# Kernel optimization log

Measured on AMD Instinct MI355X. Metric: run time of the kernel, lower is better.

The kernel has to match this reference:

```python
import jax, jax.numpy as jnp
import numpy as np
from jax import lax
import math

B, T, CIN, H, W = 8, 64, 2, 64, 64
HID, SPK_C = 32, 64
D_MODEL, N_LAYERS, D_STATE, D_CONV = 512, 4, 16, 4
D_INNER = 2 * D_MODEL
DT_RANK = math.ceil(D_MODEL / 16)  # 32
NUM_CLASSES = 11
FEAT = SPK_C * (H // 4) * (W // 4)  # 16384
BETA, THR = 0.9, 1.0

# --- surrogate-gradient spike (snntorch fast_sigmoid, slope=25) ---
@jax.custom_vjp
def spike_fn(x):
    return (x > 0).astype(x.dtype)

def _spike_fwd(x):
    return spike_fn(x), x

def _spike_bwd(x, g):
    return (g / (25.0 * jnp.abs(x) + 1.0) ** 2,)

spike_fn.defvjp(_spike_fwd, _spike_bwd)

def lif(cur, mem):
    # snntorch Leaky, reset_mechanism='subtract': reset from previous mem (detached)
    reset = lax.stop_gradient((mem > THR).astype(mem.dtype))
    mem = BETA * mem + cur - reset * THR
    spk = spike_fn(mem - THR)
    return spk, mem

def conv2d(x, w, b):
    y = lax.conv_general_dilated(x, w, (1, 1), 'SAME', dimension_numbers=('NCHW', 'OIHW', 'NCHW'))
    return y + b[None, :, None, None]

def maxpool2(x):
    return lax.reduce_window(x, -jnp.inf, lax.max, (1, 1, 2, 2), (1, 1, 2, 2), 'VALID')

def layernorm(x, w, b):
    mu = x.mean(-1, keepdims=True)
    var = ((x - mu) ** 2).mean(-1, keepdims=True)
    return (x - mu) * lax.rsqrt(var + 1e-5) * w + b

def frontend(x, c1w, c1b, c2w, c2b, c3w, c3b):
    mem1 = jnp.zeros((B, HID, H // 2, W // 2), x.dtype)
    mem2 = jnp.zeros((B, HID, H // 4, W // 4), x.dtype)
    mem3 = jnp.zeros((B, SPK_C, H // 4, W // 4), x.dtype)
    def step(carry, xt):
        m1, m2, m3 = carry
        s1, m1 = lif(maxpool2(conv2d(xt, c1w, c1b)), m1)
        s2, m2 = lif(maxpool2(conv2d(s1, c2w, c2b)), m2)
        s3, m3 = lif(conv2d(s2, c3w, c3b), m3)
        return (m1, m2, m3), s3
    _, spk = lax.scan(step, (mem1, mem2, mem3), jnp.swapaxes(x, 0, 1))
    return jnp.swapaxes(spk, 0, 1)  # (B,T,SPK_C,H/4,W/4)

def rate_smooth(a):
    # depthwise conv1d over time with kernel ones(5)/5, padding=2 (moving average)
    Tn = a.shape[1]
    ap = jnp.pad(a, ((0, 0), (2, 2), (0, 0)))
    return sum(ap[:, k:k + Tn, :] for k in range(5)) / 5.0

def mamba_block(x, p):
    ln_w, ln_b, in_w, conv_w, xproj_w, dt_w, dt_b, A_log, Dp, out_w = p
    h = layernorm(x, ln_w, ln_b)
    xr = h @ in_w  # (B,L,2*D_INNER)
    xi, res = jnp.split(xr, 2, axis=-1)
    L = xi.shape[1]
    # causal depthwise conv1d (pad D_CONV-1 left, truncate to L)
    xp = jnp.pad(xi, ((0, 0), (D_CONV - 1, 0), (0, 0)))
    xc = sum(conv_w[:, k] * xp[:, k:k + L, :] for k in range(D_CONV))
    xc = jax.nn.silu(xc)
    x_dbl = xc @ xproj_w  # (B,L,DT_RANK+2*D_STATE)
    dt = x_dbl[..., :DT_RANK]
    Bm = x_dbl[..., DT_RANK:DT_RANK + D_STATE]
    Cm = x_dbl[..., DT_RANK + D_STATE:]
    dt = jax.nn.softplus(dt @ dt_w + dt_b)  # (B,L,D_INNER)
    A = -jnp.exp(A_log)  # (D_INNER,D_STATE)
    dA = jnp.exp(dt[..., None] * A)  # (B,L,D_INNER,D_STATE)
    dBu = dt[..., None] * Bm[:, :, None, :] * xc[..., None]
    def step(hst, inp):
        dA_t, dBu_t, C_t = inp
        hst = dA_t * hst + dBu_t
        return hst, jnp.einsum('bdn,bn->bd', hst, C_t)
    h0 = jnp.zeros((x.shape[0], D_INNER, D_STATE), x.dtype)
    _, ys = lax.scan(step, h0, (jnp.swapaxes(dA, 0, 1), jnp.swapaxes(dBu, 0, 1), jnp.swapaxes(Cm, 0, 1)))
    y = jnp.swapaxes(ys, 0, 1) + xc * Dp
    y = y * jax.nn.silu(res)
    return x + y @ out_w

def _forward(x, c1w, c1b, c2w, c2b, c3w, c3b, inp_w, inp_b, ln_w, ln_b, in_w, conv_w, xproj_w, dt_w, dt_b, A_log, Dp, mb_out_w, fn_w, fn_b, cls_w, cls_b):
    spikes = frontend(x, c1w, c1b, c2w, c2b, c3w, c3b)
    act = rate_smooth(spikes.reshape(B, T, -1))
    h = act @ inp_w + inp_b
    def layer(c, p):
        return mamba_block(c, p), None
    h, _ = lax.scan(layer, h, (ln_w, ln_b, in_w, conv_w, xproj_w, dt_w, dt_b, A_log, Dp, mb_out_w))
    h = h.mean(axis=1)
    h = layernorm(h, fn_w, fn_b)
    return h @ cls_w + cls_b

def setup_inputs():
    key = jax.random.key(0)
    ks = jax.random.split(key, 16)
    def gn(k, shape, scale):
        return jax.random.normal(k, shape, jnp.float32) * scale
    x = jax.random.uniform(ks[0], (B, T, CIN, H, W), jnp.float32)
    c1w = gn(ks[1], (HID, CIN, 3, 3), 1.0 / np.sqrt(CIN * 9)); c1b = jnp.zeros((HID,))
    c2w = gn(ks[2], (HID, HID, 3, 3), 1.0 / np.sqrt(HID * 9)); c2b = jnp.zeros((HID,))
    c3w = gn(ks[3], (SPK_C, HID, 3, 3), 1.0 / np.sqrt(HID * 9)); c3b = jnp.zeros((SPK_C,))
    inp_w = gn(ks[4], (FEAT, D_MODEL), 1.0 / np.sqrt(FEAT)); inp_b = jnp.zeros((D_MODEL,))
    ln_w = jnp.ones((N_LAYERS, D_MODEL)); ln_b = jnp.zeros((N_LAYERS, D_MODEL))
    in_w = gn(ks[5], (N_LAYERS, D_MODEL, 2 * D_INNER), 1.0 / np.sqrt(D_MODEL))
    conv_w = gn(ks[6], (N_LAYERS, D_INNER, D_CONV), 1.0 / np.sqrt(D_CONV))
    xproj_w = gn(ks[7], (N_LAYERS, D_INNER, DT_RANK + 2 * D_STATE), 1.0 / np.sqrt(D_INNER))
    dt_w = gn(ks[8], (N_LAYERS, DT_RANK, D_INNER), 1.0 / np.sqrt(DT_RANK))
    dtv = jnp.exp(jax.random.uniform(ks[9], (N_LAYERS, D_INNER)) * (np.log(0.1) - np.log(0.001)) + np.log(0.001))
    dt_b = dtv + jnp.log(-jnp.expm1(-dtv))
    A_log = jnp.log(jnp.broadcast_to(jnp.arange(1, D_STATE + 1, dtype=jnp.float32), (N_LAYERS, D_INNER, D_STATE))) + jnp.zeros((N_LAYERS, D_INNER, D_STATE))
    Dp = jnp.ones((N_LAYERS, D_INNER))
    mb_out_w = gn(ks[10], (N_LAYERS, D_INNER, D_MODEL), 1.0 / np.sqrt(D_INNER))
    fn_w = jnp.ones((D_MODEL,)); fn_b = jnp.zeros((D_MODEL,))
    cls_w = gn(ks[11], (D_MODEL, NUM_CLASSES), 1.0 / np.sqrt(D_MODEL)); cls_b = jnp.zeros((NUM_CLASSES,))
    return dict(x=x, c1w=c1w, c1b=c1b, c2w=c2w, c2b=c2b, c3w=c3w, c3b=c3b, inp_w=inp_w, inp_b=inp_b, ln_w=ln_w, ln_b=ln_b, in_w=in_w, conv_w=conv_w, xproj_w=xproj_w, dt_w=dt_w, dt_b=dt_b, A_log=A_log, Dp=Dp, mb_out_w=mb_out_w, fn_w=fn_w, fn_b=fn_b, cls_w=cls_w, cls_b=cls_b)

def reference(x, c1w, c1b, c2w, c2b, c3w, c3b, inp_w, inp_b, ln_w, ln_b, in_w, conv_w, xproj_w, dt_w, dt_b, A_log, Dp, mb_out_w, fn_w, fn_b, cls_w, cls_b):
    return _forward(x, c1w, c1b, c2w, c2b, c3w, c3b, inp_w, inp_b, ln_w, ln_b, in_w, conv_w, xproj_w, dt_w, dt_b, A_log, Dp, mb_out_w, fn_w, fn_b, cls_w, cls_b)
```

## Files before the change

### kernel.cpp

```cpp
#include <hip/hip_runtime.h>
#include <math.h>


static constexpr int TT = 64;
static constexpr float BETA = 0.9f, THR = 1.0f;


__global__ __launch_bounds__(256) void k_conv1pool(const float* __restrict__ x,
    const float* __restrict__ w, const float* __restrict__ bias, float* __restrict__ out)
{
    __shared__ float sI[2 * 66 * 76];
    __shared__ float sW[576];
    const int bt = blockIdx.x;
    const int tid = threadIdx.x;
    for (int i = tid; i < 2 * 66 * 76; i += 256) sI[i] = 0.f;
    for (int i = tid; i < 576; i += 256) sW[i] = w[i];
    __syncthreads();
    const float* img = x + (size_t)bt * 8192;
    for (int i = tid; i < 2048; i += 256) {
        float4 v4 = ((const float4*)img)[i];
        int lin = i * 4;
        int ci = lin >> 12, rc = lin & 4095;
        int r = rc >> 6, c = rc & 63;
        *(float4*)&sI[ci * 5016 + (r + 1) * 76 + (c + 4)] = v4;
    }
    __syncthreads();
    const int oh = tid >> 3;
    const int p8 = (tid & 7) * 8;
    float v[2][4][10];
    #pragma unroll
    for (int ci = 0; ci < 2; ++ci) {
        #pragma unroll
        for (int dr = 0; dr < 4; ++dr) {
            const float* rp = &sI[ci * 5016 + (2 * oh + dr) * 76 + p8];
            float2 a  = *(const float2*)&rp[2];
            float4 b4 = *(const float4*)&rp[4];
            float4 c4 = *(const float4*)&rp[8];
            float2 e  = *(const float2*)&rp[12];
            v[ci][dr][0] = a.y;
            v[ci][dr][1] = b4.x; v[ci][dr][2] = b4.y; v[ci][dr][3] = b4.z; v[ci][dr][4] = b4.w;
            v[ci][dr][5] = c4.x; v[ci][dr][6] = c4.y; v[ci][dr][7] = c4.z; v[ci][dr][8] = c4.w;
            v[ci][dr][9] = e.x;
        }
    }
    const int ow0 = (tid & 7) * 4;
    float* obase = out + (size_t)bt * 32768;
    for (int co = 0; co < 32; ++co) {
        float pos[2][8];
        #pragma unroll
        for (int i = 0; i < 2; ++i)
            #pragma unroll
            for (int j = 0; j < 8; ++j) pos[i][j] = 0.f;
        #pragma unroll
        for (int ci = 0; ci < 2; ++ci) {
            const float* wp = &sW[(co * 2 + ci) * 9];
            float w0=wp[0],w1=wp[1],w2=wp[2],w3=wp[3],w4=wp[4],w5=wp[5],w6=wp[6],w7=wp[7],w8=wp[8];
            #pragma unroll
            for (int pr = 0; pr < 2; ++pr)
                #pragma unroll
                for (int pc = 0; pc < 8; ++pc)
                    pos[pr][pc] += v[ci][pr][pc]*w0 + v[ci][pr][pc+1]*w1 + v[ci][pr][pc+2]*w2
                                 + v[ci][pr+1][pc]*w3 + v[ci][pr+1][pc+1]*w4 + v[ci][pr+1][pc+2]*w5
                                 + v[ci][pr+2][pc]*w6 + v[ci][pr+2][pc+1]*w7 + v[ci][pr+2][pc+2]*w8;
        }
        float b0 = bias[co];
        float4 o;
        o.x = fmaxf(fmaxf(pos[0][0], pos[0][1]), fmaxf(pos[1][0], pos[1][1])) + b0;
        o.y = fmaxf(fmaxf(pos[0][2], pos[0][3]), fmaxf(pos[1][2], pos[1][3])) + b0;
        o.z = fmaxf(fmaxf(pos[0][4], pos[0][5]), fmaxf(pos[1][4], pos[1][5])) + b0;
        o.w = fmaxf(fmaxf(pos[0][6], pos[0][7]), fmaxf(pos[1][6], pos[1][7])) + b0;
        *(float4*)&obase[co * 1024 + oh * 32 + ow0] = o;
    }
}

__global__ __launch_bounds__(256) void k_lif(const float* __restrict__ cur,
                                             float* __restrict__ spk, int chw)
{
    int idx = blockIdx.x * 256 + threadIdx.x;
    int b = idx / chw, p = idx % chw;
    const float* cp = cur + (size_t)b * TT * chw + p;
    float* sp = spk + (size_t)b * TT * chw + p;
    float m = 0.f;
    for (int t = 0; t < TT; ++t) {
        float c = cp[(size_t)t * chw];
        float reset = (m > THR) ? THR : 0.f;
        m = BETA * m + c - reset;
        sp[(size_t)t * chw] = (m > THR) ? 1.f : 0.f;
    }
}

__global__ __launch_bounds__(256) void k_conv2(const float* __restrict__ s1,
    const float* __restrict__ w, const float* __restrict__ bias, float* __restrict__ out)
{
    __shared__ float sI[8 * 34 * 40];
    __shared__ float sWc[576];
    const int bt = blockIdx.x;
    const int co0 = blockIdx.y * 8;
    const int tid = threadIdx.x;
    for (int i = tid; i < 8 * 34 * 40; i += 256) sI[i] = 0.f;
    const int cop = (tid >> 6) * 2;
    const int lane = tid & 63;
    const int ph0 = (lane >> 3) * 4;
    const int pw0 = (lane & 7) * 4;
    float acc[2][4][4] = {};
    const float* img = s1 + (size_t)bt * 32768;
    for (int chunk = 0; chunk < 4; ++chunk) {
        __syncthreads();
        const float* src = img + chunk * 8192;
        for (int i = tid; i < 2048; i += 256) {
            float4 v4 = ((const float4*)src)[i];
            int lin = i * 4;
            int ci = lin >> 10, rc = lin & 1023;
            int r = rc >> 5, c = rc & 31;
            *(float4*)&sI[ci * 1360 + (r + 1) * 40 + (c + 4)] = v4;
        }
        for (int i = tid; i < 576; i += 256) {
            int col = i / 72, rest = i % 72;
            sWc[i] = w[(co0 + col) * 288 + chunk * 72 + rest];
        }
        __syncthreads();
        #pragma unroll
        for (int ci = 0; ci < 8; ++ci) {
            float wA[9], wB[9];
            #pragma unroll
            for (int j = 0; j < 9; ++j) {
                wA[j] = sWc[cop * 72 + ci * 9 + j];
                wB[j] = sWc[(cop + 1) * 72 + ci * 9 + j];
            }
            const float* sp = &sI[ci * 1360];
            float v[6][6];
            #pragma unroll
            for (int r6 = 0; r6 < 6; ++r6) {
                const float* rp = sp + (ph0 + r6) * 40 + pw0;
                float2 a  = *(const float2*)&rp[2];
                float4 b4 = *(const float4*)&rp[4];
                float2 e  = *(const float2*)&rp[8];
                v[r6][0] = a.y;
                v[r6][1] = b4.x; v[r6][2] = b4.y; v[r6][3] = b4.z; v[r6][4] = b4.w;
                v[r6][5] = e.x;
            }
            #pragma unroll
            for (int i = 0; i < 4; ++i)
                #pragma unroll
                for (int j = 0; j < 4; ++j) {
                    acc[0][i][j] += v[i][j]*wA[0] + v[i][j+1]*wA[1] + v[i][j+2]*wA[2]
                                  + v[i+1][j]*wA[3] + v[i+1][j+1]*wA[4] + v[i+1][j+2]*wA[5]
                                  + v[i+2][j]*wA[6] + v[i+2][j+1]*wA[7] + v[i+2][j+2]*wA[8];
                    acc[1][i][j] += v[i][j]*wB[0] + v[i][j+1]*wB[1] + v[i][j+2]*wB[2]
                                  + v[i+1][j]*wB[3] + v[i+1][j+1]*wB[4] + v[i+1][j+2]*wB[5]
                                  + v[i+2][j]*wB[6] + v[i+2][j+1]*wB[7] + v[i+2][j+2]*wB[8];
                }
        }
    }
    #pragma unroll
    for (int u = 0; u < 2; ++u) {
        int co = co0 + cop + u;
        float b0 = bias[co];
        float* ob = out + (size_t)bt * 8192 + co * 256;
        #pragma unroll
        for (int i = 0; i < 2; ++i) {
            float2 o;
            o.x = fmaxf(fmaxf(acc[u][2*i][0], acc[u][2*i][1]),
                        fmaxf(acc[u][2*i+1][0], acc[u][2*i+1][1])) + b0;
            o.y = fmaxf(fmaxf(acc[u][2*i][2], acc[u][2*i][3]),
                        fmaxf(acc[u][2*i+1][2], acc[u][2*i+1][3])) + b0;
            *(float2*)&ob[(ph0 / 2 + i) * 16 + pw0 / 2] = o;
        }
    }
}

__global__ __launch_bounds__(256) void k_conv3(const float* __restrict__ s2,
    const float* __restrict__ w, const float* __restrict__ bias, float* __restrict__ out)
{
    __shared__ float sI[32 * 16 * 17];
    __shared__ float sW[32 * 16 * 9];
    const int bt = blockIdx.x;
    const int co0 = blockIdx.y * 32;
    const int tid = threadIdx.x;
    const float* img = s2 + (size_t)bt * 8192;
    for (int i = tid; i < 2048; i += 256) {
        float4 v4 = ((const float4*)img)[i];
        int lin = i * 4;
        int ci = lin >> 8, rc = lin & 255;
        int r = rc >> 4, c = rc & 15;
        float* dst = &sI[ci * 272 + r * 17 + c];
        dst[0] = v4.x; dst[1] = v4.y; dst[2] = v4.z; dst[3] = v4.w;
    }
    const int cop = (tid >> 4) * 2;
    const int l16 = tid & 15;
    const int ph0 = (l16 >> 2) * 4;
    const int pw0 = (l16 & 3) * 4;
    float acc[2][4][4] = {};
    for (int chunk = 0; chunk < 2; ++chunk) {
        __syncthreads();
        for (int i = tid; i < 4608; i += 256) {
            int col = i / 144;
            int rest = i % 144;
            sW[i] = w[((co0 + col) * 32 + chunk * 16) * 9 + rest];
        }
        __syncthreads();
        for (int ci = 0; ci < 16; ++ci) {
            float v[6][6];
            const float* sp = &sI[(chunk * 16 + ci) * 272];
            #pragma unroll
            for (int dr = 0; dr < 6; ++dr) {
                int r = ph0 - 1 + dr;
                bool rok = (r >= 0) && (r < 16);
                #pragma unroll
                for (int dc = 0; dc < 6; ++dc) {
                    int c = pw0 - 1 + dc;
                    v[dr][dc] = (rok && c >= 0 && c < 16) ? sp[r * 17 + c] : 0.f;
                }
            }
            #pragma unroll
            for (int u = 0; u < 2; ++u) {
                const float* wp = &sW[((cop + u) * 16 + ci) * 9];
                float w0=wp[0],w1=wp[1],w2=wp[2],w3=wp[3],w4=wp[4],w5=wp[5],w6=wp[6],w7=wp[7],w8=wp[8];
                #pragma unroll
                for (int i = 0; i < 4; ++i)
                    #pragma unroll
                    for (int j = 0; j < 4; ++j)
                        acc[u][i][j] += v[i][j]*w0 + v[i][j+1]*w1 + v[i][j+2]*w2
                                      + v[i+1][j]*w3 + v[i+1][j+1]*w4 + v[i+1][j+2]*w5
                                      + v[i+2][j]*w6 + v[i+2][j+1]*w7 + v[i+2][j+2]*w8;
            }
        }
    }
    #pragma unroll
    for (int u = 0; u < 2; ++u) {
        int co = co0 + cop + u;
        float b0 = bias[co];
        float* ob = out + (size_t)bt * 16384 + co * 256;
        #pragma unroll
        for (int i = 0; i < 4; ++i) {
            float4 o;
            o.x = acc[u][i][0] + b0; o.y = acc[u][i][1] + b0;
            o.z = acc[u][i][2] + b0; o.w = acc[u][i][3] + b0;
            *(float4*)&ob[(ph0 + i) * 16 + pw0] = o;
        }
    }
}

__global__ __launch_bounds__(256) void k_lif3smooth(const float* __restrict__ cur,
                                                    float* __restrict__ act)
{
    int idx = blockIdx.x * 256 + threadIdx.x;
    int b = idx >> 14, f = idx & 16383;
    const float* cp = cur + (size_t)b * TT * 16384 + f;
    float* ap = act + (size_t)b * TT * 16384 + f;
    float m = 0.f;
    float s0 = 0, s1 = 0, s2 = 0, s3 = 0, s4 = 0;
    for (int t = 0; t < TT + 2; ++t) {
        float s = 0.f;
        if (t < TT) {
            float cv = cp[(size_t)t * 16384];
            float reset = (m > THR) ? THR : 0.f;
            m = BETA * m + cv - reset;
            s = (m > THR) ? 1.f : 0.f;
        }
        s4 = s3; s3 = s2; s2 = s1; s1 = s0; s0 = s;
        if (t >= 2) ap[(size_t)(t - 2) * 16384] = (s0 + s1 + s2 + s3 + s4) * 0.2f;
    }
}


__global__ __launch_bounds__(256) void k_gemm(const float* __restrict__ A,
    const float* __restrict__ Bm, float* __restrict__ C, int M, int N, int K)
{
    __shared__ float As[16][68];
    __shared__ float Bs[16][68];
    const int tid = threadIdx.x;
    const int n0 = blockIdx.x * 64, m0 = blockIdx.y * 64;
    const int kchunk = K / gridDim.z;
    const int k0 = blockIdx.z * kchunk, k1 = k0 + kchunk;
    const int ar = tid >> 2, ac = (tid & 3) * 4;
    const int br = tid >> 4, bc = (tid & 15) * 4;
    const int row0 = (tid >> 4) * 4, col0 = (tid & 15) * 4;
    float acc[4][4] = {};
    float4 av = *(const float4*)&A[(size_t)(m0 + ar) * K + k0 + ac];
    float4 bv = *(const float4*)&Bm[(size_t)(k0 + br) * N + n0 + bc];
    for (int kk = k0; kk < k1; kk += 16) {
        As[ac + 0][ar] = av.x; As[ac + 1][ar] = av.y;
        As[ac + 2][ar] = av.z; As[ac + 3][ar] = av.w;
        *(float4*)&Bs[br][bc] = bv;
        __syncthreads();
        if (kk + 16 < k1) {
            av = *(const float4*)&A[(size_t)(m0 + ar) * K + kk + 16 + ac];
            bv = *(const float4*)&Bm[(size_t)(kk + 16 + br) * N + n0 + bc];
        }
        #pragma unroll
        for (int k = 0; k < 16; ++k) {
            float4 a4 = *(const float4*)&As[k][row0];
            float4 b4 = *(const float4*)&Bs[k][col0];
            acc[0][0] += a4.x * b4.x; acc[0][1] += a4.x * b4.y; acc[0][2] += a4.x * b4.z; acc[0][3] += a4.x * b4.w;
            acc[1][0] += a4.y * b4.x; acc[1][1] += a4.y * b4.y; acc[1][2] += a4.y * b4.z; acc[1][3] += a4.y * b4.w;
            acc[2][0] += a4.z * b4.x; acc[2][1] += a4.z * b4.y; acc[2][2] += a4.z * b4.z; acc[2][3] += a4.z * b4.w;
            acc[3][0] += a4.w * b4.x; acc[3][1] += a4.w * b4.y; acc[3][2] += a4.w * b4.z; acc[3][3] += a4.w * b4.w;
        }
        __syncthreads();
    }
    float* Cp = C + (size_t)blockIdx.z * M * N;
    #pragma unroll
    for (int i = 0; i < 4; ++i) {
        float4 o;
        o.x = acc[i][0]; o.y = acc[i][1]; o.z = acc[i][2]; o.w = acc[i][3];
        *(float4*)&Cp[(size_t)(m0 + row0 + i) * N + n0 + col0] = o;
    }
}

template <bool ADD, bool BIAS>
__global__ __launch_bounds__(256) void k_reduce(const float* __restrict__ part,
    const float* __restrict__ bias, float* __restrict__ out, int MN, int N, int KS)
{
    int i4 = (blockIdx.x * 256 + threadIdx.x) * 4;
    if (i4 >= MN) return;
    float4 v = {0.f, 0.f, 0.f, 0.f};
    for (int z = 0; z < KS; ++z) {
        float4 p = *(const float4*)&part[(size_t)z * MN + i4];
        v.x += p.x; v.y += p.y; v.z += p.z; v.w += p.w;
    }
    if (BIAS) {
        float4 bv = *(const float4*)&bias[i4 % N];
        v.x += bv.x; v.y += bv.y; v.z += bv.z; v.w += bv.w;
    }
    if (ADD) {
        float4 o = *(const float4*)&out[i4];
        v.x += o.x; v.y += o.y; v.z += o.z; v.w += o.w;
    }
    *(float4*)&out[i4] = v;
}


__device__ __forceinline__ float blockSum(float v, float* red)
{
    #pragma unroll
    for (int o = 32; o; o >>= 1) v += __shfl_down(v, o, 64);
    const int wv = threadIdx.x >> 6, lane = threadIdx.x & 63;
    if (lane == 0) red[wv] = v;
    __syncthreads();
    float r = red[0] + red[1] + red[2] + red[3];
    __syncthreads();
    return r;
}

__global__ __launch_bounds__(256) void k_ln(const float* __restrict__ x,
    const float* __restrict__ w, const float* __restrict__ b, float* __restrict__ out)
{
    __shared__ float red[4];
    int row = blockIdx.x;
    const float* xp = x + (size_t)row * 512;
    int c = threadIdx.x * 2;
    float2 v = *(const float2*)&xp[c];
    float mu = blockSum(v.x + v.y, red) * (1.f / 512.f);
    float d0 = v.x - mu, d1 = v.y - mu;
    float var = blockSum(d0 * d0 + d1 * d1, red) * (1.f / 512.f);
    float inv = rsqrtf(var + 1e-5f);
    float2 o;
    o.x = d0 * inv * w[c] + b[c];
    o.y = d1 * inv * w[c + 1] + b[c + 1];
    *(float2*)&out[(size_t)row * 512 + c] = o;
}

__global__ __launch_bounds__(256) void k_convsilu(const float* __restrict__ xr,
    const float* __restrict__ cw, float* __restrict__ xc)
{
    int idx = blockIdx.x * 256 + threadIdx.x;
    int row = idx >> 10;
    int d = idx & 1023;
    int t = row & 63;
    const float* xi = xr + (size_t)(row - t) * 2048 + d;
    float4 w = *(const float4*)&cw[d * 4];
    float a = w.w * xi[(size_t)t * 2048];
    if (t >= 1) a += w.z * xi[(size_t)(t - 1) * 2048];
    if (t >= 2) a += w.y * xi[(size_t)(t - 2) * 2048];
    if (t >= 3) a += w.x * xi[(size_t)(t - 3) * 2048];
    xc[idx] = a / (1.f + __expf(-a));
}

__global__ __launch_bounds__(256) void k_xproj(const float* __restrict__ xc,
    const float* __restrict__ w, float* __restrict__ xdbl)
{
    int row = blockIdx.x * 4 + (threadIdx.x >> 6);
    int col = threadIdx.x & 63;
    const float* a = xc + (size_t)row * 1024;
    float acc = 0.f;
    #pragma unroll 4
    for (int k = 0; k < 1024; k += 4) {
        float4 av = *(const float4*)&a[k];
        acc += av.x * w[(size_t)k * 64 + col] + av.y * w[(size_t)(k + 1) * 64 + col]
             + av.z * w[(size_t)(k + 2) * 64 + col] + av.w * w[(size_t)(k + 3) * 64 + col];
    }
    xdbl[(size_t)row * 64 + col] = acc;
}

__global__ __launch_bounds__(256) void k_dtproj(const float* __restrict__ xdbl,
    const float* __restrict__ w, const float* __restrict__ bias, float* __restrict__ dt)
{
    int idx = blockIdx.x * 256 + threadIdx.x;
    int row = idx >> 10, d = idx & 1023;
    const float* a = xdbl + (size_t)row * 64;
    float acc = bias[d];
    #pragma unroll 8
    for (int r = 0; r < 32; ++r) acc += a[r] * w[(size_t)r * 1024 + d];
    dt[idx] = fmaxf(acc, 0.f) + log1pf(__expf(-fabsf(acc)));
}

__global__ __launch_bounds__(64) void k_scan(const float* __restrict__ dt,
    const float* __restrict__ xc, const float* __restrict__ xdbl,
    const float* __restrict__ xr, const float* __restrict__ A_log,
    const float* __restrict__ Dp, float* __restrict__ y)
{
    int idx = blockIdx.x * 64 + threadIdx.x;
    int b = idx >> 10, d = idx & 1023;
    float A[16];
    #pragma unroll
    for (int n = 0; n < 16; ++n) A[n] = -__expf(A_log[d * 16 + n]);
    float Dv = Dp[d];
    float h[16] = {};
    const int row0 = b * 64;
    size_t base = (size_t)row0 * 1024 + d;
    float dtv = dt[base], xv = xc[base];
    float res = xr[(size_t)row0 * 2048 + 1024 + d];
    const float4* Bp = (const float4*)&xdbl[(size_t)row0 * 64 + 32];
    const float4* Cq = (const float4*)&xdbl[(size_t)row0 * 64 + 48];
    float4 B0 = Bp[0], B1 = Bp[1], B2 = Bp[2], B3 = Bp[3];
    float4 C0 = Cq[0], C1 = Cq[1], C2 = Cq[2], C3 = Cq[3];
    for (int t = 0; t < TT; ++t) {
        float dtv_n = 0.f, xv_n = 0.f, res_n = 0.f;
        float4 B0n = {}, B1n = {}, B2n = {}, B3n = {}, C0n = {}, C1n = {}, C2n = {}, C3n = {};
        if (t < TT - 1) {
            size_t b2 = base + (size_t)(t + 1) * 1024;
            dtv_n = dt[b2]; xv_n = xc[b2];
            res_n = xr[(size_t)(row0 + t + 1) * 2048 + 1024 + d];
            const float4* Bp2 = (const float4*)&xdbl[(size_t)(row0 + t + 1) * 64 + 32];
            const float4* Cq2 = (const float4*)&xdbl[(size_t)(row0 + t + 1) * 64 + 48];
            B0n = Bp2[0]; B1n = Bp2[1]; B2n = Bp2[2]; B3n = Bp2[3];
            C0n = Cq2[0]; C1n = Cq2[1]; C2n = Cq2[2]; C3n = Cq2[3];
        }
        float dtx = dtv * xv;
        float acc = 0.f;
        #define SCAN_STEP(Bv, Cv, n0)                                             \
        {                                                                         \
            float bb[4] = {Bv.x, Bv.y, Bv.z, Bv.w};                               \
            float cv[4] = {Cv.x, Cv.y, Cv.z, Cv.w};                               \
            _Pragma("unroll")                                                     \
            for (int r = 0; r < 4; ++r) {                                         \
                int n = n0 + r;                                                   \
                float hv = __expf(dtv * A[n]) * h[n] + dtx * bb[r];               \
                h[n] = hv;                                                        \
                acc += hv * cv[r];                                                \
            }                                                                     \
        }
        SCAN_STEP(B0, C0, 0) SCAN_STEP(B1, C1, 4) SCAN_STEP(B2, C2, 8) SCAN_STEP(B3, C3, 12)
        #undef SCAN_STEP
        float sil = res / (1.f + __expf(-res));
        y[(size_t)(row0 + t) * 1024 + d] = (acc + xv * Dv) * sil;
        dtv = dtv_n; xv = xv_n; res = res_n;
        B0 = B0n; B1 = B1n; B2 = B2n; B3 = B3n;
        C0 = C0n; C1 = C1n; C2 = C2n; C3 = C3n;
    }
}

__global__ __launch_bounds__(256) void k_meant(const float* __restrict__ h,
                                               float* __restrict__ hm)
{
    int idx = blockIdx.x * 256 + threadIdx.x;
    int b = idx >> 9, d = idx & 511;
    const float* p = h + (size_t)b * 64 * 512 + d;
    float s = 0.f;
    for (int t = 0; t < 64; ++t) s += p[t * 512];
    hm[idx] = s * (1.f / 64.f);
}

__global__ __launch_bounds__(256) void k_final(const float* __restrict__ hm,
    const float* __restrict__ fw, const float* __restrict__ fb,
    const float* __restrict__ cw, const float* __restrict__ cb, float* __restrict__ out)
{
    __shared__ float red[4];
    __shared__ float nrm[512];
    int b = blockIdx.x;
    const float* xp = hm + (size_t)b * 512;
    int c2 = threadIdx.x * 2;
    float2 v = *(const float2*)&xp[c2];
    float mu = blockSum(v.x + v.y, red) * (1.f / 512.f);
    float d0 = v.x - mu, d1 = v.y - mu;
    float var = blockSum(d0 * d0 + d1 * d1, red) * (1.f / 512.f);
    float inv = rsqrtf(var + 1e-5f);
    nrm[c2] = d0 * inv * fw[c2] + fb[c2];
    nrm[c2 + 1] = d1 * inv * fw[c2 + 1] + fb[c2 + 1];
    __syncthreads();
    for (int c = 0; c < 11; ++c) {
        float p = nrm[threadIdx.x] * cw[threadIdx.x * 11 + c]
                + nrm[threadIdx.x + 256] * cw[(threadIdx.x + 256) * 11 + c];
        float s = blockSum(p, red);
        if (threadIdx.x == 0) out[b * 11 + c] = s + cb[c];
    }
}


extern "C" void kernel_launch(void* const* d_in, const int* in_sizes, int n_in,
                              void* d_out, int out_size, void* d_ws, size_t ws_size,
                              hipStream_t stream)
{
    const float* x      = (const float*)d_in[0];
    const float* c1w    = (const float*)d_in[1];
    const float* c1b    = (const float*)d_in[2];
    const float* c2w    = (const float*)d_in[3];
    const float* c2b    = (const float*)d_in[4];
    const float* c3w    = (const float*)d_in[5];
    const float* c3b    = (const float*)d_in[6];
    const float* inp_w  = (const float*)d_in[7];
    const float* inp_b  = (const float*)d_in[8];
    const float* ln_w   = (const float*)d_in[9];
    const float* ln_b   = (const float*)d_in[10];
    const float* in_w   = (const float*)d_in[11];
    const float* conv_w = (const float*)d_in[12];
    const float* xproj_w= (const float*)d_in[13];
    const float* dt_w   = (const float*)d_in[14];
    const float* dt_b   = (const float*)d_in[15];
    const float* A_log  = (const float*)d_in[16];
    const float* Dp     = (const float*)d_in[17];
    const float* mb_out_w=(const float*)d_in[18];
    const float* fn_w   = (const float*)d_in[19];
    const float* fn_b   = (const float*)d_in[20];
    const float* cls_w  = (const float*)d_in[21];
    const float* cls_b  = (const float*)d_in[22];
    float* out = (float*)d_out;

    float* ws   = (float*)d_ws;
    float* bufA = ws;
    float* bufB = bufA + 16777216;
    float* h    = bufB + 16777216;
    float* hn   = h    + 262144;
    float* xr   = hn   + 262144;
    float* xc   = xr   + 1048576;
    float* xdbl = xc   + 524288;
    float* dtb  = xdbl + 32768;
    float* yb   = dtb  + 524288;
    float* hm   = yb   + 524288;

    k_conv1pool<<<512, 256, 0, stream>>>(x, c1w, c1b, bufA);
    k_lif<<<1024, 256, 0, stream>>>(bufA, bufB, 32768);
    k_conv2<<<dim3(512, 4), 256, 0, stream>>>(bufB, c2w, c2b, bufA);
    k_lif<<<256, 256, 0, stream>>>(bufA, bufB, 8192);
    k_conv3<<<dim3(512, 2), 256, 0, stream>>>(bufB, c3w, c3b, bufA);
    k_lif3smooth<<<512, 256, 0, stream>>>(bufA, bufB);

    k_gemm<<<dim3(8, 8, 32), 256, 0, stream>>>(bufB, inp_w, bufA, 512, 512, 16384);
    k_reduce<false, true><<<256, 256, 0, stream>>>(bufA, inp_b, h, 262144, 512, 32);

    for (int l = 0; l < 4; ++l) {
        k_ln<<<512, 256, 0, stream>>>(h, ln_w + l * 512, ln_b + l * 512, hn);
        k_gemm<<<dim3(32, 8, 8), 256, 0, stream>>>(hn, in_w + (size_t)l * 1048576, bufA, 512, 2048, 512);
        k_reduce<false, false><<<1024, 256, 0, stream>>>(bufA, nullptr, xr, 1048576, 2048, 8);
        k_convsilu<<<2048, 256, 0, stream>>>(xr, conv_w + l * 4096, xc);
        k_xproj<<<128, 256, 0, stream>>>(xc, xproj_w + l * 65536, xdbl);
        k_dtproj<<<2048, 256, 0, stream>>>(xdbl, dt_w + l * 32768, dt_b + l * 1024, dtb);
        k_scan<<<128, 64, 0, stream>>>(dtb, xc, xdbl, xr, A_log + l * 16384, Dp + l * 1024, yb);
        k_gemm<<<dim3(8, 8, 16), 256, 0, stream>>>(yb, mb_out_w + (size_t)l * 524288, bufA, 512, 512, 1024);
        k_reduce<true, false><<<256, 256, 0, stream>>>(bufA, nullptr, h, 262144, 512, 16);
    }

    k_meant<<<16, 256, 0, stream>>>(h, hm);
    k_final<<<8, 256, 0, stream>>>(hm, fn_w, fn_b, cls_w, cls_b, out);
}
```

Measured before the change: 1.122 ms.

## Restructure conv2/conv3 thread mapping to one pixel per thread with smaller smem

Conv2 now has each thread compute four pre-pool pixels across all eight output channels, loads all weights once up front and stages input in smaller 4-channel chunks. The 2x2 max-pool is done with cross-lane shuffles. Conv3 switches to one output pixel per thread over 16 channels, with a zero-padded input tile (no bounds checks), float4-aligned padded weights and twice as many blocks. Both kernels declare higher occupancy. The aim is less register pressure and branching and better occupancy, at the cost of more redundant input reads per FMA and scalar output stores.

```diff
diff --git a/kernel.cpp b/kernel.cpp
--- a/kernel.cpp
+++ b/kernel.cpp
@@ -89,156 +89,128 @@
     }
 }
 
-__global__ __launch_bounds__(256) void k_conv2(const float* __restrict__ s1,
+__global__ __launch_bounds__(256, 4) void k_conv2(const float* __restrict__ s1,
     const float* __restrict__ w, const float* __restrict__ bias, float* __restrict__ out)
 {
-    __shared__ float sI[8 * 34 * 40];
-    __shared__ float sWc[576];
+    __shared__ float sI[4 * 34 * 40];
+    __shared__ float sW[8 * 32 * 9];
     const int bt = blockIdx.x;
     const int co0 = blockIdx.y * 8;
     const int tid = threadIdx.x;
-    for (int i = tid; i < 8 * 34 * 40; i += 256) sI[i] = 0.f;
-    const int cop = (tid >> 6) * 2;
-    const int lane = tid & 63;
-    const int ph0 = (lane >> 3) * 4;
-    const int pw0 = (lane & 7) * 4;
-    float acc[2][4][4] = {};
+    for (int i = tid; i < 4 * 34 * 40; i += 256) sI[i] = 0.f;
+    for (int i = tid; i < 2304; i += 256) {
+        int col = i / 288, rest = i % 288;
+        sW[i] = w[(co0 + col) * 288 + rest];
+    }
+    const int cc = tid & 31;
+    const int r0 = tid >> 5;
+    float acc[8][4] = {};
     const float* img = s1 + (size_t)bt * 32768;
-    for (int chunk = 0; chunk < 4; ++chunk) {
+    for (int chunk = 0; chunk < 8; ++chunk) {
         __syncthreads();
-        const float* src = img + chunk * 8192;
-        for (int i = tid; i < 2048; i += 256) {
+        const float* src = img + chunk * 4096;
+        for (int i = tid; i < 1024; i += 256) {
             float4 v4 = ((const float4*)src)[i];
             int lin = i * 4;
             int ci = lin >> 10, rc = lin & 1023;
             int r = rc >> 5, c = rc & 31;
             *(float4*)&sI[ci * 1360 + (r + 1) * 40 + (c + 4)] = v4;
         }
-        for (int i = tid; i < 576; i += 256) {
-            int col = i / 72, rest = i % 72;
-            sWc[i] = w[(co0 + col) * 288 + chunk * 72 + rest];
-        }
         __syncthreads();
         #pragma unroll
-        for (int ci = 0; ci < 8; ++ci) {
-            float wA[9], wB[9];
+        for (int ci4 = 0; ci4 < 4; ++ci4) {
+            float win[4][9];
             #pragma unroll
-            for (int j = 0; j < 9; ++j) {
-                wA[j] = sWc[cop * 72 + ci * 9 + j];
-                wB[j] = sWc[(cop + 1) * 72 + ci * 9 + j];
-            }
-            const float* sp = &sI[ci * 1360];
-            float v[6][6];
-            #pragma unroll
-            for (int r6 = 0; r6 < 6; ++r6) {
-                const float* rp = sp + (ph0 + r6) * 40 + pw0;
-                float2 a  = *(const float2*)&rp[2];
-                float4 b4 = *(const float4*)&rp[4];
-                float2 e  = *(const float2*)&rp[8];
-                v[r6][0] = a.y;
-                v[r6][1] = b4.x; v[r6][2] = b4.y; v[r6][3] = b4.z; v[r6][4] = b4.w;
-                v[r6][5] = e.x;
-            }
-            #pragma unroll
-            for (int i = 0; i < 4; ++i)
+            for (int p = 0; p < 4; ++p) {
+                const float* sp = &sI[ci4 * 1360 + (r0 + 8 * p) * 40 + cc + 3];
                 #pragma unroll
-                for (int j = 0; j < 4; ++j) {
-                    acc[0][i][j] += v[i][j]*wA[0] + v[i][j+1]*wA[1] + v[i][j+2]*wA[2]
-                                  + v[i+1][j]*wA[3] + v[i+1][j+1]*wA[4] + v[i+1][j+2]*wA[5]
-                                  + v[i+2][j]*wA[6] + v[i+2][j+1]*wA[7] + v[i+2][j+2]*wA[8];
-                    acc[1][i][j] += v[i][j]*wB[0] + v[i][j+1]*wB[1] + v[i][j+2]*wB[2]
-                                  + v[i+1][j]*wB[3] + v[i+1][j+1]*wB[4] + v[i+1][j+2]*wB[5]
-                                  + v[i+2][j]*wB[6] + v[i+2][j+1]*wB[7] + v[i+2][j+2]*wB[8];
-                }
-        }
-    }
-    #pragma unroll
-    for (int u = 0; u < 2; ++u) {
-        int co = co0 + cop + u;
-        float b0 = bias[co];
-        float* ob = out + (size_t)bt * 8192 + co * 256;
-        #pragma unroll
-        for (int i = 0; i < 2; ++i) {
-            float2 o;
-            o.x = fmaxf(fmaxf(acc[u][2*i][0], acc[u][2*i][1]),
-                        fmaxf(acc[u][2*i+1][0], acc[u][2*i+1][1])) + b0;
-            o.y = fmaxf(fmaxf(acc[u][2*i][2], acc[u][2*i][3]),
-                        fmaxf(acc[u][2*i+1][2], acc[u][2*i+1][3])) + b0;
-            *(float2*)&ob[(ph0 / 2 + i) * 16 + pw0 / 2] = o;
-        }
-    }
-}
-
-__global__ __launch_bounds__(256) void k_conv3(const float* __restrict__ s2,
-    const float* __restrict__ w, const float* __restrict__ bias, float* __restrict__ out)
-{
-    __shared__ float sI[32 * 16 * 17];
-    __shared__ float sW[32 * 16 * 9];
-    const int bt = blockIdx.x;
-    const int co0 = blockIdx.y * 32;
-    const int tid = threadIdx.x;
-    const float* img = s2 + (size_t)bt * 8192;
-    for (int i = tid; i < 2048; i += 256) {
-        float4 v4 = ((const float4*)img)[i];
-        int lin = i * 4;
-        int ci = lin >> 8, rc = lin & 255;
-        int r = rc >> 4, c = rc & 15;
-        float* dst = &sI[ci * 272 + r * 17 + c];
-        dst[0] = v4.x; dst[1] = v4.y; dst[2] = v4.z; dst[3] = v4.w;
-    }
-    const int cop = (tid >> 4) * 2;
-    const int l16 = tid & 15;
-    const int ph0 = (l16 >> 2) * 4;
-    const int pw0 = (l16 & 3) * 4;
-    float acc[2][4][4] = {};
-    for (int chunk = 0; chunk < 2; ++chunk) {
-        __syncthreads();
-        for (int i = tid; i < 4608; i += 256) {
-            int col = i / 144;
-            int rest = i % 144;
-            sW[i] = w[((co0 + col) * 32 + chunk * 16) * 9 + rest];
-        }
-        __syncthreads();
-        for (int ci = 0; ci < 16; ++ci) {
-            float v[6][6];
-            const float* sp = &sI[(chunk * 16 + ci) * 272];
-            #pragma unroll
-            for (int dr = 0; dr < 6; ++dr) {
-                int r = ph0 - 1 + dr;
-                bool rok = (r >= 0) && (r < 16);
-                #pragma unroll
-                for (int dc = 0; dc < 6; ++dc) {
-                    int c = pw0 - 1 + dc;
-                    v[dr][dc] = (rok && c >= 0 && c < 16) ? sp[r * 17 + c] : 0.f;
+                for (int j = 0; j < 3; ++j) {
+                    win[p][3*j+0] = sp[j * 40 + 0];
+                    win[p][3*j+1] = sp[j * 40 + 1];
+                    win[p][3*j+2] = sp[j * 40 + 2];
                 }
             }
             #pragma unroll
-            for (int u = 0; u < 2; ++u) {
-                const float* wp = &sW[((cop + u) * 16 + ci) * 9];
+            for (int co = 0; co < 8; ++co) {
+                const float* wp = &sW[(co * 32 + chunk * 4 + ci4) * 9];
                 float w0=wp[0],w1=wp[1],w2=wp[2],w3=wp[3],w4=wp[4],w5=wp[5],w6=wp[6],w7=wp[7],w8=wp[8];
                 #pragma unroll
-                for (int i = 0; i < 4; ++i)
-                    #pragma unroll
-                    for (int j = 0; j < 4; ++j)
-                        acc[u][i][j] += v[i][j]*w0 + v[i][j+1]*w1 + v[i][j+2]*w2
-                                      + v[i+1][j]*w3 + v[i+1][j+1]*w4 + v[i+1][j+2]*w5
-                                      + v[i+2][j]*w6 + v[i+2][j+1]*w7 + v[i+2][j+2]*w8;
+                for (int p = 0; p < 4; ++p)
+                    acc[co][p] += win[p][0]*w0 + win[p][1]*w1 + win[p][2]*w2
+                                + win[p][3]*w3 + win[p][4]*w4 + win[p][5]*w5
+                                + win[p][6]*w6 + win[p][7]*w7 + win[p][8]*w8;
             }
         }
     }
+    const int lane = tid & 63;
+    const int wv = tid >> 6;
+    const bool writer = (lane & 33) == 0;
     #pragma unroll
-    for (int u = 0; u < 2; ++u) {
-        int co = co0 + cop + u;
-        float b0 = bias[co];
-        float* ob = out + (size_t)bt * 16384 + co * 256;
-        #pragma unroll
-        for (int i = 0; i < 4; ++i) {
-            float4 o;
-            o.x = acc[u][i][0] + b0; o.y = acc[u][i][1] + b0;
-            o.z = acc[u][i][2] + b0; o.w = acc[u][i][3] + b0;
-            *(float4*)&ob[(ph0 + i) * 16 + pw0] = o;
-        }
-    }
+    for (int co = 0; co < 8; ++co) {
+        float b0 = bias[co0 + co];
+        float* ob = out + (size_t)bt * 8192 + (co0 + co) * 256;
+        #pragma unroll
+        for (int p = 0; p < 4; ++p) {
+            float v = acc[co][p];
+            v = fmaxf(v, __shfl_xor(v, 1, 64));
+            v = fmaxf(v, __shfl_xor(v, 32, 64));
+            if (writer) ob[(wv + 4 * p) * 16 + (lane >> 1)] = v + b0;
+        }
+    }
+}
+
+__global__ __launch_bounds__(256, 4) void k_conv3(const float* __restrict__ s2,
+    const float* __restrict__ w, const float* __restrict__ bias, float* __restrict__ out)
+{
+    __shared__ float sI[8 * 18 * 24];
+    __shared__ float sW3[8 * 16 * 12];
+    const int bt = blockIdx.x;
+    const int co0 = blockIdx.y * 16;
+    const int tid = threadIdx.x;
+    for (int i = tid; i < 8 * 18 * 24; i += 256) sI[i] = 0.f;
+    const int rr = tid >> 4;
+    const int cc = tid & 15;
+    float acc[16] = {};
+    const float* img = s2 + (size_t)bt * 8192;
+    for (int chunk = 0; chunk < 4; ++chunk) {
+        __syncthreads();
+        const float* src = img + chunk * 2048;
+        for (int i = tid; i < 512; i += 256) {
+            float4 v4 = ((const float4*)src)[i];
+            int lin = i * 4;
+            int ci = lin >> 8, rc = lin & 255;
+            int r = rc >> 4, c = rc & 15;
+            *(float4*)&sI[ci * 432 + (r + 1) * 24 + (c + 4)] = v4;
+        }
+        for (int i = tid; i < 1152; i += 256) {
+            int ci = i / 144, rest = i % 144;
+            int co = rest / 9, k = rest % 9;
+            sW3[(ci * 16 + co) * 12 + k] = w[(co0 + co) * 288 + (chunk * 8 + ci) * 9 + k];
+        }
+        __syncthreads();
+        #pragma unroll
+        for (int ci = 0; ci < 8; ++ci) {
+            float v0,v1,v2,v3,v4,v5,v6,v7,v8;
+            {
+                const float* sp = &sI[ci * 432 + rr * 24 + cc + 3];
+                v0 = sp[0];  v1 = sp[1];  v2 = sp[2];
+                v3 = sp[24]; v4 = sp[25]; v5 = sp[26];
+                v6 = sp[48]; v7 = sp[49]; v8 = sp[50];
+            }
+            #pragma unroll
+            for (int co = 0; co < 16; ++co) {
+                const float4* wq = (const float4*)&sW3[(ci * 16 + co) * 12];
+                float4 wa = wq[0], wb = wq[1], wc = wq[2];
+                acc[co] += v0*wa.x + v1*wa.y + v2*wa.z
+                         + v3*wa.w + v4*wb.x + v5*wb.y
+                         + v6*wb.z + v7*wb.w + v8*wc.x;
+            }
+        }
+    }
+    float* ob = out + (size_t)bt * 16384 + rr * 16 + cc;
+    #pragma unroll
+    for (int co = 0; co < 16; ++co)
+        ob[(co0 + co) * 256] = acc[co] + bias[co0 + co];
 }
 
 __global__ __launch_bounds__(256) void k_lif3smooth(const float* __restrict__ cur,
@@ -543,7 +515,7 @@
     k_lif<<<1024, 256, 0, stream>>>(bufA, bufB, 32768);
     k_conv2<<<dim3(512, 4), 256, 0, stream>>>(bufB, c2w, c2b, bufA);
     k_lif<<<256, 256, 0, stream>>>(bufA, bufB, 8192);
-    k_conv3<<<dim3(512, 2), 256, 0, stream>>>(bufB, c3w, c3b, bufA);
+    k_conv3<<<dim3(512, 4), 256, 0, stream>>>(bufB, c3w, c3b, bufA);
     k_lif3smooth<<<512, 256, 0, stream>>>(bufA, bufB);
 
     k_gemm<<<dim3(8, 8, 32), 256, 0, stream>>>(bufB, inp_w, bufA, 512, 512, 16384);
```

Measured after the change: 1.567 ms. 39.6% more time.
